# Optimization experiments

Measured on AMD Instinct MI355X. Metric: run time of the kernel, lower is better.

Reference implementation:

```python
import jax, jax.numpy as jnp
import numpy as np

D_MODEL = 1024
N_HEAD = 16
HEAD_DIM = D_MODEL // N_HEAD
B, S = 4, 2048


def setup_inputs() -> dict:
    key = jax.random.key(0)
    ks = jax.random.split(key, 11)
    s = 1.0 / np.sqrt(D_MODEL)
    return {
        "query": jax.random.normal(ks[0], (B, S, D_MODEL), jnp.float32),
        "key": jax.random.normal(ks[1], (B, S, D_MODEL), jnp.float32),
        "value": jax.random.normal(ks[2], (B, S, D_MODEL), jnp.float32),
        "Wq": jax.random.normal(ks[3], (D_MODEL, D_MODEL), jnp.float32) * s,
        "bq": jax.random.normal(ks[4], (D_MODEL,), jnp.float32) * s,
        "Wk": jax.random.normal(ks[5], (D_MODEL, D_MODEL), jnp.float32) * s,
        "bk": jax.random.normal(ks[6], (D_MODEL,), jnp.float32) * s,
        "Wv": jax.random.normal(ks[7], (D_MODEL, D_MODEL), jnp.float32) * s,
        "bv": jax.random.normal(ks[8], (D_MODEL,), jnp.float32) * s,
        "Wo": jax.random.normal(ks[9], (D_MODEL, D_MODEL), jnp.float32) * s,
        "bo": jax.random.normal(ks[10], (D_MODEL,), jnp.float32) * s,
    }


def reference(query, key, value, Wq, bq, Wk, bk, Wv, bv, Wo, bo):
    b, s, d_model = query.shape
    # projections; reshape to [b, h, s, hd]
    def proj(x, W, bias):
        return (x @ W + bias).reshape(b, s, N_HEAD, HEAD_DIM).transpose(0, 2, 1, 3)
    q = proj(query, Wq, bq)
    k = proj(key, Wk, bk)
    v = proj(value, Wv, bv)
    # NOTE: original code scales by sqrt(d_model) (bug-faithful), not sqrt(head_dim)
    scores = jnp.einsum("bhqd,bhkd->bhqk", q, k) / jnp.sqrt(jnp.float32(d_model))
    causal = jnp.tril(jnp.ones((s, s), dtype=bool))
    scores = jnp.where(causal[None, None], scores, -jnp.inf)
    p = jax.nn.softmax(scores, axis=-1)  # dropout is identity in eval
    x = jnp.einsum("bhqk,bhkd->bhqd", p, v)
    x = x.transpose(0, 2, 1, 3).reshape(b, s, d_model)
    return x @ Wo + bo
```

## Files before the change

kernel.cpp:

```cpp
#include <hip/hip_runtime.h>
#include <hip/hip_bf16.h>
#include <cstdint>
#include <cstddef>

#define D_MODEL 1024
#define N_HEAD 16
#define HEAD_DIM 64
#define BATCH 4
#define SEQ 2048
#define M_ROWS (BATCH * SEQ)

typedef __attribute__((ext_vector_type(8))) short short8v;
typedef __attribute__((ext_vector_type(4))) float f32x4;
typedef __attribute__((ext_vector_type(16))) float f32x16;

__device__ __forceinline__ unsigned short f2bf(float f) {
    union { uint32_t i; float f; } c;
    c.f = f;
    uint32_t r = c.i + 0x7FFFu + ((c.i >> 16) & 1u);
    return (unsigned short)(r >> 16);
}
__device__ __forceinline__ unsigned short trunc_bf(float f) {
    return (unsigned short)(__float_as_uint(f) >> 16);
}
__device__ __forceinline__ uint32_t pack_trunc2(float a, float b) {
    return __builtin_amdgcn_perm(__float_as_uint(b), __float_as_uint(a), 0x07060302u);
}
__device__ __forceinline__ uint32_t pack_rne2(float a, float b) {
    return (uint32_t)f2bf(a) | ((uint32_t)f2bf(b) << 16);
}

struct __align__(16) U4 { uint32_t x, y, z, w; };
struct __align__(8) U2 { uint32_t x, y; };

__device__ __forceinline__ int sw_off(int row, int gl) {
    return row * 64 + ((gl ^ (row & 7)) << 3);
}

__device__ __forceinline__ void gload16(const unsigned short *g, unsigned short *l) {
    __builtin_amdgcn_global_load_lds((const __attribute__((address_space(1))) void *)g,
                                     (__attribute__((address_space(3))) void *)l, 16, 0, 0);
}

__global__ __launch_bounds__(256)
void cvt_kernel(const float *__restrict__ src, unsigned short *__restrict__ dst)
{
    const size_t i = ((size_t)blockIdx.x * 256 + threadIdx.x) * 8;
    float4 lo = *(const float4 *)(src + i);
    float4 hi = *(const float4 *)(src + i + 4);
    U4 pk;
    pk.x = pack_trunc2(lo.x, lo.y);
    pk.y = pack_trunc2(lo.z, lo.w);
    pk.z = pack_trunc2(hi.x, hi.y);
    pk.w = pack_trunc2(hi.z, hi.w);
    *(U4 *)(dst + i) = pk;
}

__global__ __launch_bounds__(256)
void wtrans_kernel(const float *__restrict__ W, unsigned short *__restrict__ Wt)
{
    __shared__ float tile[32][33];
    const int t = threadIdx.x;
    const int tx = t & 31, ty = t >> 5;
    const int bk = blockIdx.y * 32, bn = blockIdx.x * 32;
#pragma unroll
    for (int i = 0; i < 4; i++)
        tile[ty + 8 * i][tx] = W[(size_t)(bk + ty + 8 * i) * D_MODEL + bn + tx];
    __syncthreads();
#pragma unroll
    for (int i = 0; i < 4; i++)
        Wt[(size_t)(bn + ty + 8 * i) * D_MODEL + bk + tx] = trunc_bf(tile[tx][ty + 8 * i]);
}

template <typename TA, int MODE, typename TO>
__global__ __launch_bounds__(256, 2)
void mgemm_kernel(const TA *__restrict__ A,
                  const unsigned short *__restrict__ Wt,
                  const float *__restrict__ bias,
                  TO *__restrict__ out,
                  float escale)
{
    __shared__ __align__(16) unsigned short At[128 * 64];
    __shared__ __align__(16) unsigned short Bt[128 * 64];

    const int t = threadIdx.x;
    const int wave = t >> 6;
    const int lane = t & 63;
    const int n_ = lane & 15;
    const int quad = lane >> 4;
    const int wm = wave >> 1, wn = wave & 1;
    const int m0 = blockIdx.x * 128;
    const int n0 = blockIdx.y * 128;

    f32x4 acc[4][4];
#pragma unroll
    for (int i = 0; i < 4; i++)
#pragma unroll
        for (int j = 0; j < 4; j++) acc[i][j] = (f32x4){0.f, 0.f, 0.f, 0.f};

    const int srow = t >> 3;
    const int sg = t & 7;
    const int rl = lane >> 3;
    const int gsw = (lane & 7) ^ rl;

    for (int k0 = 0; k0 < D_MODEL; k0 += 64) {
        __syncthreads();
        if constexpr (sizeof(TA) == 2) {
            const unsigned short *Ab = (const unsigned short *)A;
#pragma unroll
            for (int c = 0; c < 4; c++) {
                const int rb = wave * 32 + c * 8;
                gload16(Ab + (size_t)(m0 + rb + rl) * D_MODEL + k0 + (gsw << 3), &At[rb * 64]);
                gload16(Wt + (size_t)(n0 + rb + rl) * D_MODEL + k0 + (gsw << 3), &Bt[rb * 64]);
            }
        } else {
#pragma unroll
            for (int i = 0; i < 4; i++) {
                const int r = srow + 32 * i;
                const float *p = (const float *)A + (size_t)(m0 + r) * D_MODEL + k0 + sg * 8;
                float4 lo = *(const float4 *)p;
                float4 hi = *(const float4 *)(p + 4);
                U4 pk;
                pk.x = pack_trunc2(lo.x, lo.y);
                pk.y = pack_trunc2(lo.z, lo.w);
                pk.z = pack_trunc2(hi.x, hi.y);
                pk.w = pack_trunc2(hi.z, hi.w);
                *(U4 *)&At[sw_off(r, sg)] = pk;
            }
#pragma unroll
            for (int i = 0; i < 4; i++) {
                const int r = srow + 32 * i;
                const unsigned short *p = Wt + (size_t)(n0 + r) * D_MODEL + k0 + sg * 8;
                *(U4 *)&Bt[sw_off(r, sg)] = *(const U4 *)p;
            }
        }
        __syncthreads();

#pragma unroll
        for (int c = 0; c < 2; c++) {
            short8v af[4], bf[4];
#pragma unroll
            for (int mt = 0; mt < 4; mt++)
                af[mt] = *(const short8v *)&At[sw_off(wm * 64 + mt * 16 + n_, c * 4 + quad)];
#pragma unroll
            for (int nt = 0; nt < 4; nt++)
                bf[nt] = *(const short8v *)&Bt[sw_off(wn * 64 + nt * 16 + n_, c * 4 + quad)];
#pragma unroll
            for (int mt = 0; mt < 4; mt++)
#pragma unroll
                for (int nt = 0; nt < 4; nt++)
                    acc[mt][nt] = __builtin_amdgcn_mfma_f32_16x16x32_bf16(
                        af[mt], bf[nt], acc[mt][nt], 0, 0, 0);
        }
    }

    float bi[4];
#pragma unroll
    for (int nt = 0; nt < 4; nt++) bi[nt] = bias[n0 + wn * 64 + nt * 16 + n_];

    if constexpr (MODE == 2) {
#pragma unroll
        for (int mt = 0; mt < 4; mt++) {
            const int m = m0 + wm * 64 + mt * 16 + quad * 4;
#pragma unroll
            for (int nt = 0; nt < 4; nt++) {
                const int col = n0 + wn * 64 + nt * 16 + n_;
                const size_t idx = ((size_t)(m >> 11) * D_MODEL + col) * SEQ + (m & 2047);
                U2 pk;
                pk.x = pack_rne2(acc[mt][nt][0] + bi[nt], acc[mt][nt][1] + bi[nt]);
                pk.y = pack_rne2(acc[mt][nt][2] + bi[nt], acc[mt][nt][3] + bi[nt]);
                *(U2 *)((unsigned short *)out + idx) = pk;
            }
        }
    } else {
#pragma unroll
        for (int mt = 0; mt < 4; mt++)
#pragma unroll
            for (int reg = 0; reg < 4; reg++) {
                const int m = m0 + wm * 64 + mt * 16 + quad * 4 + reg;
#pragma unroll
                for (int nt = 0; nt < 4; nt++) {
                    const int col = n0 + wn * 64 + nt * 16 + n_;
                    const float v = (acc[mt][nt][reg] + bi[nt]) * escale;
                    if constexpr (MODE == 1)
                        ((unsigned short *)out)[(size_t)m * D_MODEL + col] = f2bf(v);
                    else
                        ((float *)out)[(size_t)m * D_MODEL + col] = v;
                }
            }
    }
}

__global__ __launch_bounds__(256, 2)
void attn_kernel(const unsigned short *Qg,
                 const unsigned short *__restrict__ Kg,
                 const unsigned short *__restrict__ VTg,
                 unsigned short *AO)
{
    __shared__ __align__(16) unsigned short Kt[64 * 64];
    __shared__ __align__(16) unsigned short Vt[64 * 64];

    const int h = blockIdx.x;
    const int b = blockIdx.y;
    const int qpair = blockIdx.z;
    const int t = threadIdx.x;
    const int w = t >> 6;
    const int lane = t & 63;
    const int ql = lane & 31;
    const int hi = lane >> 5;

    const size_t row_base = (size_t)b * SEQ * D_MODEL + h * HEAD_DIM;
    const size_t vhead = (size_t)(b * N_HEAD + h) * HEAD_DIM * SEQ;

    const int r0 = t >> 3;
    const int g = t & 7;

#pragma unroll
    for (int pass = 0; pass < 2; ++pass) {
        const int qb = pass ? (15 - qpair) : qpair;
        const int qs0 = qb * 128 + w * 32;
        const int qseq = qs0 + ql;

        short8v qf[4];
#pragma unroll
        for (int c = 0; c < 4; c++)
            qf[c] = *(const short8v *)(Qg + row_base + (size_t)qseq * D_MODEL + c * 16 + hi * 8);

        float m_i = -INFINITY, l_i = 0.f;
        f32x16 Oacc[2];
#pragma unroll
        for (int dt = 0; dt < 2; dt++)
#pragma unroll
            for (int i = 0; i < 16; i++) Oacc[dt][i] = 0.f;

        const int kb_max = 2 * qb + 1;

        U4 kvA = *(const U4 *)(Kg + row_base + (size_t)r0 * D_MODEL + g * 8);
        U4 kvB = *(const U4 *)(Kg + row_base + (size_t)(r0 + 32) * D_MODEL + g * 8);
        U4 vvA = *(const U4 *)(VTg + vhead + (size_t)r0 * SEQ + g * 8);
        U4 vvB = *(const U4 *)(VTg + vhead + (size_t)(r0 + 32) * SEQ + g * 8);

        for (int kb = 0; kb <= kb_max; ++kb) {
            __syncthreads();
            *(U4 *)&Kt[sw_off(r0, g)] = kvA;
            *(U4 *)&Kt[sw_off(r0 + 32, g)] = kvB;
            *(U4 *)&Vt[sw_off(r0, g)] = vvA;
            *(U4 *)&Vt[sw_off(r0 + 32, g)] = vvB;
            __syncthreads();

            if (kb < kb_max) {
                const int kn = (kb + 1) * 64;
                kvA = *(const U4 *)(Kg + row_base + (size_t)(kn + r0) * D_MODEL + g * 8);
                kvB = *(const U4 *)(Kg + row_base + (size_t)(kn + r0 + 32) * D_MODEL + g * 8);
                vvA = *(const U4 *)(VTg + vhead + (size_t)r0 * SEQ + kn + g * 8);
                vvB = *(const U4 *)(VTg + vhead + (size_t)(r0 + 32) * SEQ + kn + g * 8);
            }
            __builtin_amdgcn_sched_barrier(0);

            if (kb * 64 > qs0 + 31) continue;

            f32x16 st[2];
            __builtin_amdgcn_s_setprio(1);
#pragma unroll
            for (int kt = 0; kt < 2; kt++) {
#pragma unroll
                for (int i = 0; i < 16; i++) st[kt][i] = 0.f;
#pragma unroll
                for (int c = 0; c < 4; c++) {
                    short8v kf = *(const short8v *)&Kt[sw_off(kt * 32 + ql, c * 2 + hi)];
                    st[kt] = __builtin_amdgcn_mfma_f32_32x32x16_bf16(kf, qf[c], st[kt], 0, 0, 0);
                }
            }
            __builtin_amdgcn_s_setprio(0);

            if (kb * 64 + 63 > qs0) {
#pragma unroll
                for (int kt = 0; kt < 2; kt++)
#pragma unroll
                    for (int r = 0; r < 16; r++) {
                        const int kseq = kb * 64 + kt * 32 + (r & 3) + 8 * (r >> 2) + 4 * hi;
                        if (kseq > qseq) st[kt][r] = -INFINITY;
                    }
            }

            float mx = -INFINITY;
#pragma unroll
            for (int kt = 0; kt < 2; kt++)
#pragma unroll
                for (int r = 0; r < 16; r++) mx = fmaxf(mx, st[kt][r]);
            mx = fmaxf(mx, __shfl_xor(mx, 32, 64));
            const float mnew = fmaxf(m_i, mx);
            const float alpha = __builtin_amdgcn_exp2f(m_i - mnew);
            m_i = mnew;
            float rs = 0.f;
#pragma unroll
            for (int kt = 0; kt < 2; kt++)
#pragma unroll
                for (int r = 0; r < 16; r++) {
                    const float p = __builtin_amdgcn_exp2f(st[kt][r] - mnew);
                    st[kt][r] = p;
                    rs += p;
                }
            rs += __shfl_xor(rs, 32, 64);
            l_i = l_i * alpha + rs;
#pragma unroll
            for (int dt = 0; dt < 2; dt++)
#pragma unroll
                for (int r = 0; r < 16; r++) Oacc[dt][r] *= alpha;

            short8v pf[4];
#pragma unroll
            for (int tt = 0; tt < 4; tt++) {
                const int kt = tt >> 1, o = (tt & 1) * 8;
                const uint32_t A  = pack_trunc2(st[kt][o + 0], st[kt][o + 1]);
                const uint32_t A2 = pack_trunc2(st[kt][o + 2], st[kt][o + 3]);
                const uint32_t B  = pack_trunc2(st[kt][o + 4], st[kt][o + 5]);
                const uint32_t B2 = pack_trunc2(st[kt][o + 6], st[kt][o + 7]);
                const uint32_t c1 = (uint32_t)__shfl_xor((int)(hi ? A : B), 32, 64);
                const uint32_t c2 = (uint32_t)__shfl_xor((int)(hi ? A2 : B2), 32, 64);
                union { uint32_t u[4]; short8v s; } cv;
                cv.u[0] = hi ? c1 : A;
                cv.u[1] = hi ? c2 : A2;
                cv.u[2] = hi ? B : c1;
                cv.u[3] = hi ? B2 : c2;
                pf[tt] = cv.s;
            }

            __builtin_amdgcn_s_setprio(1);
#pragma unroll
            for (int dt = 0; dt < 2; dt++)
#pragma unroll
                for (int tt = 0; tt < 4; tt++) {
                    short8v vf = *(const short8v *)&Vt[sw_off(dt * 32 + ql, tt * 2 + hi)];
                    Oacc[dt] = __builtin_amdgcn_mfma_f32_32x32x16_bf16(vf, pf[tt], Oacc[dt], 0, 0, 0);
                }
            __builtin_amdgcn_s_setprio(0);
        }

        const float linv = 1.f / l_i;
        const size_t obase = row_base + (size_t)qseq * D_MODEL;
#pragma unroll
        for (int dt = 0; dt < 2; dt++)
#pragma unroll
            for (int rg = 0; rg < 4; rg++) {
                const int d0 = dt * 32 + 8 * rg + 4 * hi;
                U2 pk;
                pk.x = (uint32_t)f2bf(Oacc[dt][4 * rg + 0] * linv) |
                       ((uint32_t)f2bf(Oacc[dt][4 * rg + 1] * linv) << 16);
                pk.y = (uint32_t)f2bf(Oacc[dt][4 * rg + 2] * linv) |
                       ((uint32_t)f2bf(Oacc[dt][4 * rg + 3] * linv) << 16);
                *(U2 *)(AO + obase + d0) = pk;
            }
    }
}

extern "C" void kernel_launch(void *const *d_in, const int *in_sizes, int n_in,
                              void *d_out, int out_size, void *d_ws, size_t ws_size,
                              hipStream_t stream)
{
    const float *q  = (const float *)d_in[0];
    const float *k  = (const float *)d_in[1];
    const float *v  = (const float *)d_in[2];
    const float *Wq = (const float *)d_in[3];
    const float *bq = (const float *)d_in[4];
    const float *Wk = (const float *)d_in[5];
    const float *bk = (const float *)d_in[6];
    const float *Wv = (const float *)d_in[7];
    const float *bv = (const float *)d_in[8];
    const float *Wo = (const float *)d_in[9];
    const float *bo = (const float *)d_in[10];
    float *out = (float *)d_out;

    const size_t TENS = (size_t)M_ROWS * D_MODEL;
    const size_t WT = (size_t)D_MODEL * D_MODEL;

    unsigned short *qbuf = (unsigned short *)d_ws;
    unsigned short *kbuf = qbuf + TENS;
    unsigned short *vtbuf = kbuf + TENS;
    unsigned short *cbuf = vtbuf + TENS;
    unsigned short *wt_new = cbuf + TENS;
    unsigned short *wt_old = vtbuf + TENS;

    dim3 wgrid(32, 32);
    dim3 ggrid(M_ROWS / 128, D_MODEL / 128);
    const int cgrid = (int)(TENS / 8 / 256);

    const float qscale = 0.03125f * 1.44269504088896341f;

    const size_t need_new = (5 * TENS + WT) * sizeof(unsigned short);

    if (ws_size >= need_new) {
        unsigned short *wt = wt_new;
        wtrans_kernel<<<wgrid, 256, 0, stream>>>(Wq, wt);
        cvt_kernel<<<cgrid, 256, 0, stream>>>(q, cbuf);
        mgemm_kernel<unsigned short, 1, unsigned short><<<ggrid, 256, 0, stream>>>(cbuf, wt, bq, qbuf, qscale);
        wtrans_kernel<<<wgrid, 256, 0, stream>>>(Wk, wt);
        cvt_kernel<<<cgrid, 256, 0, stream>>>(k, cbuf);
        mgemm_kernel<unsigned short, 1, unsigned short><<<ggrid, 256, 0, stream>>>(cbuf, wt, bk, kbuf, 1.f);
        wtrans_kernel<<<wgrid, 256, 0, stream>>>(Wv, wt);
        cvt_kernel<<<cgrid, 256, 0, stream>>>(v, cbuf);
        mgemm_kernel<unsigned short, 2, unsigned short><<<ggrid, 256, 0, stream>>>(cbuf, wt, bv, vtbuf, 1.f);

        attn_kernel<<<dim3(N_HEAD, BATCH, SEQ / 256), 256, 0, stream>>>(qbuf, kbuf, vtbuf, qbuf);

        wtrans_kernel<<<wgrid, 256, 0, stream>>>(Wo, wt);
        mgemm_kernel<unsigned short, 3, float><<<ggrid, 256, 0, stream>>>(qbuf, wt, bo, out, 1.f);
    } else {
        unsigned short *wt = wt_old;
        wtrans_kernel<<<wgrid, 256, 0, stream>>>(Wq, wt);
        mgemm_kernel<float, 1, unsigned short><<<ggrid, 256, 0, stream>>>(q, wt, bq, qbuf, qscale);
        wtrans_kernel<<<wgrid, 256, 0, stream>>>(Wk, wt);
        mgemm_kernel<float, 1, unsigned short><<<ggrid, 256, 0, stream>>>(k, wt, bk, kbuf, 1.f);
        wtrans_kernel<<<wgrid, 256, 0, stream>>>(Wv, wt);
        mgemm_kernel<float, 2, unsigned short><<<ggrid, 256, 0, stream>>>(v, wt, bv, vtbuf, 1.f);

        attn_kernel<<<dim3(N_HEAD, BATCH, SEQ / 256), 256, 0, stream>>>(qbuf, kbuf, vtbuf, qbuf);

        wtrans_kernel<<<wgrid, 256, 0, stream>>>(Wo, wt);
        mgemm_kernel<unsigned short, 3, float><<<ggrid, 256, 0, stream>>>(qbuf, wt, bo, out, 1.f);
    }
}
```

Measured before the change: 379.0 us.

## Double GEMM K-step to 128 and drop register prefetch in attention loop

The projection GEMM now stages two 64-wide K slices per iteration into doubled shared-memory buffers, halving the number of barrier pairs per tile at the cost of twice the LDS per block (64KB). The attention kernel's register-level prefetch of the next K/V tile is removed and replaced by synchronous load-then-store each iteration, along with the sched_barrier. That cuts register pressure but exposes global load latency inside the loop. The doubled LDS may reduce GEMM occupancy against the launch bound of 2 blocks.

```diff
diff --git a/kernel.cpp b/kernel.cpp
--- a/kernel.cpp
+++ b/kernel.cpp
@@ -80,8 +80,8 @@
                   TO *__restrict__ out,
                   float escale)
 {
-    __shared__ __align__(16) unsigned short At[128 * 64];
-    __shared__ __align__(16) unsigned short Bt[128 * 64];
+    __shared__ __align__(16) unsigned short At[2][128 * 64];
+    __shared__ __align__(16) unsigned short Bt[2][128 * 64];
 
     const int t = threadIdx.x;
     const int wave = t >> 6;
@@ -103,48 +103,58 @@
     const int rl = lane >> 3;
     const int gsw = (lane & 7) ^ rl;
 
-    for (int k0 = 0; k0 < D_MODEL; k0 += 64) {
+    for (int k0 = 0; k0 < D_MODEL; k0 += 128) {
         __syncthreads();
         if constexpr (sizeof(TA) == 2) {
             const unsigned short *Ab = (const unsigned short *)A;
 #pragma unroll
-            for (int c = 0; c < 4; c++) {
-                const int rb = wave * 32 + c * 8;
-                gload16(Ab + (size_t)(m0 + rb + rl) * D_MODEL + k0 + (gsw << 3), &At[rb * 64]);
-                gload16(Wt + (size_t)(n0 + rb + rl) * D_MODEL + k0 + (gsw << 3), &Bt[rb * 64]);
-            }
+            for (int h = 0; h < 2; h++)
+#pragma unroll
+                for (int c = 0; c < 4; c++) {
+                    const int rb = wave * 32 + c * 8;
+                    gload16(Ab + (size_t)(m0 + rb + rl) * D_MODEL + k0 + h * 64 + (gsw << 3),
+                            &At[h][rb * 64]);
+                    gload16(Wt + (size_t)(n0 + rb + rl) * D_MODEL + k0 + h * 64 + (gsw << 3),
+                            &Bt[h][rb * 64]);
+                }
         } else {
 #pragma unroll
-            for (int i = 0; i < 4; i++) {
-                const int r = srow + 32 * i;
-                const float *p = (const float *)A + (size_t)(m0 + r) * D_MODEL + k0 + sg * 8;
-                float4 lo = *(const float4 *)p;
-                float4 hi = *(const float4 *)(p + 4);
-                U4 pk;
-                pk.x = pack_trunc2(lo.x, lo.y);
-                pk.y = pack_trunc2(lo.z, lo.w);
-                pk.z = pack_trunc2(hi.x, hi.y);
-                pk.w = pack_trunc2(hi.z, hi.w);
-                *(U4 *)&At[sw_off(r, sg)] = pk;
-            }
-#pragma unroll
-            for (int i = 0; i < 4; i++) {
-                const int r = srow + 32 * i;
-                const unsigned short *p = Wt + (size_t)(n0 + r) * D_MODEL + k0 + sg * 8;
-                *(U4 *)&Bt[sw_off(r, sg)] = *(const U4 *)p;
+            for (int h = 0; h < 2; h++) {
+#pragma unroll
+                for (int i = 0; i < 4; i++) {
+                    const int r = srow + 32 * i;
+                    const float *p =
+                        (const float *)A + (size_t)(m0 + r) * D_MODEL + k0 + h * 64 + sg * 8;
+                    float4 lo = *(const float4 *)p;
+                    float4 hi = *(const float4 *)(p + 4);
+                    U4 pk;
+                    pk.x = pack_trunc2(lo.x, lo.y);
+                    pk.y = pack_trunc2(lo.z, lo.w);
+                    pk.z = pack_trunc2(hi.x, hi.y);
+                    pk.w = pack_trunc2(hi.z, hi.w);
+                    *(U4 *)&At[h][sw_off(r, sg)] = pk;
+                }
+#pragma unroll
+                for (int i = 0; i < 4; i++) {
+                    const int r = srow + 32 * i;
+                    const unsigned short *p =
+                        Wt + (size_t)(n0 + r) * D_MODEL + k0 + h * 64 + sg * 8;
+                    *(U4 *)&Bt[h][sw_off(r, sg)] = *(const U4 *)p;
+                }
             }
         }
         __syncthreads();
 
 #pragma unroll
-        for (int c = 0; c < 2; c++) {
+        for (int c = 0; c < 4; c++) {
+            const int bk_ = c >> 1, cc = c & 1;
             short8v af[4], bf[4];
 #pragma unroll
             for (int mt = 0; mt < 4; mt++)
-                af[mt] = *(const short8v *)&At[sw_off(wm * 64 + mt * 16 + n_, c * 4 + quad)];
+                af[mt] = *(const short8v *)&At[bk_][sw_off(wm * 64 + mt * 16 + n_, cc * 4 + quad)];
 #pragma unroll
             for (int nt = 0; nt < 4; nt++)
-                bf[nt] = *(const short8v *)&Bt[sw_off(wn * 64 + nt * 16 + n_, c * 4 + quad)];
+                bf[nt] = *(const short8v *)&Bt[bk_][sw_off(wn * 64 + nt * 16 + n_, cc * 4 + quad)];
 #pragma unroll
             for (int mt = 0; mt < 4; mt++)
 #pragma unroll
@@ -235,27 +245,17 @@
 
         const int kb_max = 2 * qb + 1;
 
-        U4 kvA = *(const U4 *)(Kg + row_base + (size_t)r0 * D_MODEL + g * 8);
-        U4 kvB = *(const U4 *)(Kg + row_base + (size_t)(r0 + 32) * D_MODEL + g * 8);
-        U4 vvA = *(const U4 *)(VTg + vhead + (size_t)r0 * SEQ + g * 8);
-        U4 vvB = *(const U4 *)(VTg + vhead + (size_t)(r0 + 32) * SEQ + g * 8);
-
         for (int kb = 0; kb <= kb_max; ++kb) {
             __syncthreads();
-            *(U4 *)&Kt[sw_off(r0, g)] = kvA;
-            *(U4 *)&Kt[sw_off(r0 + 32, g)] = kvB;
-            *(U4 *)&Vt[sw_off(r0, g)] = vvA;
-            *(U4 *)&Vt[sw_off(r0 + 32, g)] = vvB;
+#pragma unroll
+            for (int i = 0; i < 2; i++) {
+                const int r = r0 + 32 * i;
+                U4 kv = *(const U4 *)(Kg + row_base + (size_t)(kb * 64 + r) * D_MODEL + g * 8);
+                *(U4 *)&Kt[sw_off(r, g)] = kv;
+                U4 vv = *(const U4 *)(VTg + vhead + (size_t)r * SEQ + kb * 64 + g * 8);
+                *(U4 *)&Vt[sw_off(r, g)] = vv;
+            }
             __syncthreads();
-
-            if (kb < kb_max) {
-                const int kn = (kb + 1) * 64;
-                kvA = *(const U4 *)(Kg + row_base + (size_t)(kn + r0) * D_MODEL + g * 8);
-                kvB = *(const U4 *)(Kg + row_base + (size_t)(kn + r0 + 32) * D_MODEL + g * 8);
-                vvA = *(const U4 *)(VTg + vhead + (size_t)r0 * SEQ + kn + g * 8);
-                vvB = *(const U4 *)(VTg + vhead + (size_t)(r0 + 32) * SEQ + kn + g * 8);
-            }
-            __builtin_amdgcn_sched_barrier(0);
 
             if (kb * 64 > qs0 + 31) continue;
 
```

After: 321.4 us. 1.18x faster.
